# Optimization experiments

Measured on AMD Instinct MI355X. Metric: run time of the kernel, lower is better.

Reference implementation:

```python
import jax, jax.numpy as jnp
import numpy as np

ALPHA = 2.0    # ATan surrogate sharpness
V_TH = 1.0     # LIF firing threshold
TAU = 2.0      # LIF membrane time constant
BN_EPS = 1e-5
NUM_HEADS = 8

@jax.custom_vjp
def spike(u):
    return (u >= 0.0).astype(u.dtype)

def _spike_fwd(u):
    return spike(u), u

def _spike_bwd(u, g):
    s = (jnp.pi / 2.0) * ALPHA * u
    return (g * (ALPHA / 2.0) / (1.0 + s * s),)

spike.defvjp(_spike_fwd, _spike_bwd)

def lif(x):
    # x: (T, ...) -> binary spikes, multi-step LIF with hard reset
    def step(mem, xt):
        mem = mem + (xt - mem) / TAU
        s = spike(mem - V_TH)
        return mem * (1.0 - s), s
    _, out = jax.lax.scan(step, jnp.zeros_like(x[0]), x)
    return out

def bn_eval(y, bn):
    g, be, m, v = bn[0], bn[1], bn[2], bn[3]  # each (C,)
    return (y - m) * jax.lax.rsqrt(v + BN_EPS) * g + be

def linear_bn_lif(x, W, b, bn):
    # x: (T,B,N,C); W: (C_out, C_in) torch convention
    y = jnp.einsum('tbnc,dc->tbnd', x, W) + b
    return lif(bn_eval(y, bn))

def setup_inputs() -> dict:
    key = jax.random.key(0)
    ks = jax.random.split(key, 6)
    T, B, N, C = 4, 8, 1024, 512
    scale = 1.0 / np.sqrt(C)
    x = jax.random.normal(ks[0], (T, B, N, C), dtype=jnp.float32)
    Wq = jax.random.normal(ks[1], (C, C), dtype=jnp.float32) * scale
    Wk = jax.random.normal(ks[2], (C, C), dtype=jnp.float32) * scale
    Wv = jax.random.normal(ks[3], (C, C), dtype=jnp.float32) * scale
    Wp = jax.random.normal(ks[4], (C, C), dtype=jnp.float32) * scale
    zeros = jnp.zeros((C,), dtype=jnp.float32)
    ones = jnp.ones((C,), dtype=jnp.float32)
    # bn_params[l] = (gamma, beta, running_mean, running_var) for q_bn,k_bn,v_bn,proj_bn
    bn_one = jnp.stack([ones, zeros, zeros, ones])  # (4, C)
    bn_params = jnp.tile(bn_one[None], (4, 1, 1))   # (4, 4, C)
    return {"x": x, "Wq": Wq, "bq": zeros, "Wk": Wk, "bk": zeros,
            "Wv": Wv, "bv": zeros, "Wp": Wp, "bp": zeros, "bn_params": bn_params}

def reference(x, Wq, bq, Wk, bk, Wv, bv, Wp, bp, bn_params):
    T, B, N, C = x.shape
    H = NUM_HEADS
    D = C // H
    q = linear_bn_lif(x, Wq, bq, bn_params[0])
    k = linear_bn_lif(x, Wk, bk, bn_params[1])
    v = linear_bn_lif(x, Wv, bv, bn_params[2])
    # (T,B,N,C) -> (T,B,H,N,D)
    q = q.reshape(T, B, N, H, D).transpose(0, 1, 3, 2, 4)
    k = k.reshape(T, B, N, H, D).transpose(0, 1, 3, 2, 4)
    v = v.reshape(T, B, N, H, D).transpose(0, 1, 3, 2, 4)
    # attention_linear variant: kv = (k^T @ v) / n; y = q @ kv
    # SparseMatmul's tile-sparsity fallback computes the same dense matmul math.
    kv = jnp.einsum('tbhnd,tbhne->tbhde', k, v) / float(N)
    y = jnp.einsum('tbhnd,tbhde->tbhne', q, kv)
    y = y.transpose(0, 1, 3, 2, 4).reshape(T, B, N, C)
    y = lif(y)  # attn_lif
    # final projection: proj -> proj_bn -> proj_lif
    y = jnp.einsum('tbnc,dc->tbnd', y, Wp) + bp
    y = bn_eval(y, bn_params[3])
    y = lif(y)  # proj_lif
    return y
```

## Files before the change

### kernel.cpp

```cpp
#include <hip/hip_runtime.h>
#include <hip/hip_bf16.h>

constexpr int T_ = 4, B_ = 8, N_ = 1024, C_ = 512, H_ = 8, D_ = 64;
constexpr int M_ = 8192;
constexpr int MT_ = 32768;
constexpr int K_ = 512;

#define TAU_INV 0.5f
#define V_TH    1.0f
#define BN_EPS  1e-5f

__device__ __forceinline__ void ld4(const float* p, float* d) {
  const float4 v = *(const float4*)p;
  d[0] = v.x; d[1] = v.y; d[2] = v.z; d[3] = v.w;
}
__device__ __forceinline__ void ld4(const __hip_bfloat16* p, float* d) {
  const ushort4 u = *(const ushort4*)p;
  d[0] = __bfloat162float(*(const __hip_bfloat16*)&u.x);
  d[1] = __bfloat162float(*(const __hip_bfloat16*)&u.y);
  d[2] = __bfloat162float(*(const __hip_bfloat16*)&u.z);
  d[3] = __bfloat162float(*(const __hip_bfloat16*)&u.w);
}
__device__ __forceinline__ void st4(__hip_bfloat16* p, const float* s) {
  ushort4 u;
  *(__hip_bfloat16*)&u.x = __float2bfloat16(s[0]);
  *(__hip_bfloat16*)&u.y = __float2bfloat16(s[1]);
  *(__hip_bfloat16*)&u.z = __float2bfloat16(s[2]);
  *(__hip_bfloat16*)&u.w = __float2bfloat16(s[3]);
  *(ushort4*)p = u;
}
__device__ __forceinline__ void st4(float* p, const float* s) {
  *(float4*)p = make_float4(s[0], s[1], s[2], s[3]);
}

__device__ __forceinline__ void dma16(const void* g, void* l) {
  __builtin_amdgcn_global_load_lds(
      (const __attribute__((address_space(1))) unsigned int*)g,
      (__attribute__((address_space(3))) unsigned int*)l, 16, 0, 0);
}

struct WPtrs { const float* W[4]; };

__global__ __launch_bounds__(256) void transpose_w(WPtrs wp, float* __restrict__ Wt)
{
  __shared__ float tile[32][33];
  const int w = blockIdx.z;
  const float* __restrict__ W = wp.W[w];
  float* __restrict__ dst = Wt + (size_t)w * K_ * C_;
  const int k0 = blockIdx.x * 32, d0 = blockIdx.y * 32;
  const int tx = threadIdx.x, ty = threadIdx.y;
#pragma unroll
  for (int i = 0; i < 32; i += 8)
    tile[ty + i][tx] = W[(size_t)(d0 + ty + i) * K_ + k0 + tx];
  __syncthreads();
#pragma unroll
  for (int i = 0; i < 32; i += 8)
    dst[(size_t)(k0 + ty + i) * C_ + d0 + tx] = tile[tx][ty + i];
}

__global__ __launch_bounds__(256) void transpose_x(
    const float* __restrict__ x, float* __restrict__ XT)
{
  __shared__ float tile[32][132];
  const int bk = blockIdx.x * 32, bm = blockIdx.y * 32;
  const int tx = threadIdx.x & 31, ty = threadIdx.x >> 5;
#pragma unroll
  for (int t = 0; t < T_; ++t)
#pragma unroll
    for (int i = 0; i < 4; ++i) {
      const int m = ty + 8 * i;
      tile[tx][m * 4 + t] = x[((size_t)t * M_ + bm + m) * K_ + bk + tx];
    }
  __syncthreads();
  const int k = threadIdx.x >> 3, q = threadIdx.x & 7;
#pragma unroll
  for (int u = 0; u < 4; ++u)
    st4(&XT[(size_t)(bk + k) * MT_ + bm * 4 + q * 16 + u * 4],
        &tile[k][q * 16 + u * 4]);
}

template <typename TIn, typename TOut>
struct GArgs {
  const TIn* AT;
  const float* Wt[3];
  const float* bias[3];
  const float* bn[3];
  TOut* S[3];
};

template <typename TIn, typename TOut>
__global__ __launch_bounds__(256, 2) void gemm_lif(GArgs<TIn, TOut> args)
{
  constexpr int BK = 32;
  constexpr bool BF = (sizeof(TIn) == 2);
  __shared__ __align__(16) TIn  As[BK * 128];
  __shared__ __align__(16) float Bs[BK * 256];

  const int z = blockIdx.z;
  const TIn*   __restrict__ AT   = args.AT;
  const float* __restrict__ Wt   = args.Wt[z];
  const float* __restrict__ bias = args.bias[z];
  const float* __restrict__ bnp  = args.bn[z];
  TOut*        __restrict__ S    = args.S[z];

  const int tid  = threadIdx.x;
  const int lane = tid & 63;
  const int wave = __builtin_amdgcn_readfirstlane(tid >> 6);
  const int tx = tid & 15, ty = tid >> 4;
  const int bm_m = blockIdx.y * 32;
  const int bm4  = bm_m * 4;
  const int bn0  = blockIdx.x * 256;

  float acc[2][4][4][4];
#pragma unroll
  for (int g = 0; g < 2; ++g)
#pragma unroll
    for (int h = 0; h < 4; ++h)
#pragma unroll
      for (int i = 0; i < 4; ++i)
#pragma unroll
        for (int j = 0; j < 4; ++j) acc[g][h][i][j] = 0.0f;

  for (int k0 = 0; k0 < K_; k0 += BK) {
    if constexpr (!BF) {
#pragma unroll
      for (int c = 0; c < 4; ++c) {
        const int ins = wave * 4 + c;
        const int kk = ins * 2 + (lane >> 5);
        dma16(AT + (size_t)(k0 + kk) * MT_ + bm4 + (lane & 31) * 4,
              (void*)((float*)As + ins * 256));
      }
    } else {
#pragma unroll
      for (int c = 0; c < 2; ++c) {
        const int ins = wave * 2 + c;
        const int kk = ins * 4 + (lane >> 4);
        dma16(AT + (size_t)(k0 + kk) * MT_ + bm4 + (lane & 15) * 8,
              (void*)((TIn*)As + ins * 512));
      }
    }
#pragma unroll
    for (int c = 0; c < 8; ++c) {
      const int ins = wave * 8 + c;
      dma16(Wt + (size_t)(k0 + ins) * C_ + bn0 + lane * 4,
            (void*)(Bs + ins * 256));
    }
    __syncthreads();

#pragma unroll
    for (int kk = 0; kk < BK; ++kk) {
      float a[2][4], b[4][4];
#pragma unroll
      for (int g = 0; g < 2; ++g)
        ld4((const TIn*)As + kk * 128 + ty * 4 + 64 * g, a[g]);
#pragma unroll
      for (int h = 0; h < 4; ++h)
        ld4(Bs + kk * 256 + tx * 4 + 64 * h, b[h]);
#pragma unroll
      for (int g = 0; g < 2; ++g)
#pragma unroll
        for (int h = 0; h < 4; ++h)
#pragma unroll
          for (int i = 0; i < 4; ++i)
#pragma unroll
            for (int j = 0; j < 4; ++j)
              acc[g][h][i][j] += a[g][i] * b[h][j];
    }
    __syncthreads();
  }

#pragma unroll
  for (int h = 0; h < 4; ++h) {
    const int d = bn0 + tx * 4 + 64 * h;
    float bi[4], gg[4], be[4], mu[4], vv[4];
    ld4(&bias[d], bi);
    ld4(&bnp[d], gg);
    ld4(&bnp[C_ + d], be);
    ld4(&bnp[2 * C_ + d], mu);
    ld4(&bnp[3 * C_ + d], vv);
    float inv[4];
#pragma unroll
    for (int j = 0; j < 4; ++j) inv[j] = 1.0f / sqrtf(vv[j] + BN_EPS);
#pragma unroll
    for (int g = 0; g < 2; ++g) {
      const int m = bm_m + ty + 16 * g;
      float sv[4][4];
#pragma unroll
      for (int j = 0; j < 4; ++j) {
        float mm = 0.0f;
#pragma unroll
        for (int t = 0; t < 4; ++t) {
          float y = acc[g][h][t][j] + bi[j];
          y = (y - mu[j]) * inv[j] * gg[j] + be[j];
          float m2 = mm + (y - mm) * TAU_INV;
          float s = (m2 - V_TH >= 0.0f) ? 1.0f : 0.0f;
          sv[t][j] = s;
          mm = (s != 0.0f) ? 0.0f : m2;
        }
      }
#pragma unroll
      for (int t = 0; t < 4; ++t)
        st4(&S[((size_t)t * M_ + m) * C_ + d], sv[t]);
    }
  }
}

__global__ __launch_bounds__(256) void lif_T(
    const float* __restrict__ Y, __hip_bfloat16* __restrict__ AT)
{
  __shared__ __hip_bfloat16 lds[64][72];
  const int bm = blockIdx.x * 16, bc = blockIdx.y * 64;
  const int tid = threadIdx.x;
  const int mm = tid >> 4, c4 = (tid & 15) * 4;
  float mem[4] = {0.0f, 0.0f, 0.0f, 0.0f};
#pragma unroll
  for (int t = 0; t < T_; ++t) {
    float y[4];
    ld4(&Y[((size_t)t * M_ + bm + mm) * C_ + bc + c4], y);
#pragma unroll
    for (int j = 0; j < 4; ++j) {
      float m2 = mem[j] + (y[j] - mem[j]) * TAU_INV;
      float s = (m2 - V_TH >= 0.0f) ? 1.0f : 0.0f;
      lds[c4 + j][mm * 4 + t] = __float2bfloat16(s);
      mem[j] = (s != 0.0f) ? 0.0f : m2;
    }
  }
  __syncthreads();
  const int c = tid >> 2, q = tid & 3;
  *(uint4*)(AT + (size_t)(bc + c) * MT_ + bm * 4 + q * 16) =
      *(const uint4*)&lds[c][q * 16];
}

__global__ __launch_bounds__(256) void attn_kernel(
    const __hip_bfloat16* __restrict__ Q,
    const __hip_bfloat16* __restrict__ Kk,
    const __hip_bfloat16* __restrict__ V,
    float* __restrict__ Y)
{
  __shared__ float s1[64][65];
  __shared__ float s2[64][65];
  __shared__ float kv[64][65];
  const int tid = threadIdx.x;
  const int h = blockIdx.x, b = blockIdx.y, t = blockIdx.z;
  const size_t base = ((size_t)t * B_ + b) * (size_t)N_ * C_ + (size_t)h * D_;
  const int d0 = (tid >> 4) * 4;
  const int e0 = (tid & 15) * 4;

  float acc[4][4];
#pragma unroll
  for (int i = 0; i < 4; ++i)
#pragma unroll
    for (int j = 0; j < 4; ++j) acc[i][j] = 0.0f;

  for (int nc = 0; nc < N_; nc += 64) {
#pragma unroll
    for (int i = 0; i < 16; ++i) {
      int idx = tid + i * 256;
      int r = idx >> 6, c = idx & 63;
      s1[r][c] = __bfloat162float(Kk[base + (size_t)(nc + r) * C_ + c]);
      s2[r][c] = __bfloat162float(V[base + (size_t)(nc + r) * C_ + c]);
    }
    __syncthreads();
#pragma unroll
    for (int nn = 0; nn < 64; ++nn) {
      float a[4], bb[4];
#pragma unroll
      for (int i = 0; i < 4; ++i) a[i] = s1[nn][d0 + i];
#pragma unroll
      for (int j = 0; j < 4; ++j) bb[j] = s2[nn][e0 + j];
#pragma unroll
      for (int i = 0; i < 4; ++i)
#pragma unroll
        for (int j = 0; j < 4; ++j) acc[i][j] += a[i] * bb[j];
    }
    __syncthreads();
  }
#pragma unroll
  for (int i = 0; i < 4; ++i)
#pragma unroll
    for (int j = 0; j < 4; ++j)
      kv[d0 + i][e0 + j] = acc[i][j] * (1.0f / (float)N_);
  __syncthreads();

  for (int rc = 0; rc < N_; rc += 64) {
#pragma unroll
    for (int i = 0; i < 16; ++i) {
      int idx = tid + i * 256;
      int r = idx >> 6, c = idx & 63;
      s1[r][c] = __bfloat162float(Q[base + (size_t)(rc + r) * C_ + c]);
    }
    __syncthreads();
    float o[4][4];
#pragma unroll
    for (int i = 0; i < 4; ++i)
#pragma unroll
      for (int j = 0; j < 4; ++j) o[i][j] = 0.0f;
#pragma unroll
    for (int d = 0; d < 64; ++d) {
      float a[4], bb[4];
#pragma unroll
      for (int i = 0; i < 4; ++i) a[i] = s1[d0 + i][d];
#pragma unroll
      for (int j = 0; j < 4; ++j) bb[j] = kv[d][e0 + j];
#pragma unroll
      for (int i = 0; i < 4; ++i)
#pragma unroll
        for (int j = 0; j < 4; ++j) o[i][j] += a[i] * bb[j];
    }
#pragma unroll
    for (int i = 0; i < 4; ++i)
#pragma unroll
      for (int j = 0; j < 4; ++j)
        Y[base + (size_t)(rc + d0 + i) * C_ + e0 + j] = o[i][j];
    __syncthreads();
  }
}

extern "C" void kernel_launch(void* const* d_in, const int* in_sizes, int n_in,
                              void* d_out, int out_size, void* d_ws, size_t ws_size,
                              hipStream_t stream)
{
  const float* x   = (const float*)d_in[0];
  const float* Wq  = (const float*)d_in[1];
  const float* bq  = (const float*)d_in[2];
  const float* Wk  = (const float*)d_in[3];
  const float* bk  = (const float*)d_in[4];
  const float* Wv  = (const float*)d_in[5];
  const float* bv  = (const float*)d_in[6];
  const float* Wp  = (const float*)d_in[7];
  const float* bp  = (const float*)d_in[8];
  const float* bnp = (const float*)d_in[9];
  float* out = (float*)d_out;

  char* ws = (char*)d_ws;
  float* XT = (float*)ws;  ws += (size_t)K_ * MT_ * sizeof(float);
  float* Wt = (float*)ws;  ws += (size_t)4 * K_ * C_ * sizeof(float);
  __hip_bfloat16* q_s = (__hip_bfloat16*)ws; ws += (size_t)MT_ * C_ * 2;
  __hip_bfloat16* k_s = (__hip_bfloat16*)ws; ws += (size_t)MT_ * C_ * 2;
  __hip_bfloat16* v_s = (__hip_bfloat16*)ws; ws += (size_t)MT_ * C_ * 2;
  float* Y = XT;
  __hip_bfloat16* aT = q_s;

  WPtrs wp; wp.W[0] = Wq; wp.W[1] = Wk; wp.W[2] = Wv; wp.W[3] = Wp;
  transpose_w<<<dim3(K_ / 32, C_ / 32, 4), dim3(32, 8), 0, stream>>>(wp, Wt);
  transpose_x<<<dim3(K_ / 32, M_ / 32), 256, 0, stream>>>(x, XT);

  GArgs<float, __hip_bfloat16> qa;
  qa.AT = XT;
  qa.Wt[0] = Wt; qa.Wt[1] = Wt + (size_t)K_ * C_; qa.Wt[2] = Wt + (size_t)2 * K_ * C_;
  qa.bias[0] = bq; qa.bias[1] = bk; qa.bias[2] = bv;
  qa.bn[0] = bnp + 0 * 4 * C_;
  qa.bn[1] = bnp + 1 * 4 * C_;
  qa.bn[2] = bnp + 2 * 4 * C_;
  qa.S[0] = q_s; qa.S[1] = k_s; qa.S[2] = v_s;
  gemm_lif<float, __hip_bfloat16>
      <<<dim3(C_ / 256, M_ / 32, 3), 256, 0, stream>>>(qa);

  attn_kernel<<<dim3(H_, B_, T_), 256, 0, stream>>>(q_s, k_s, v_s, Y);
  lif_T<<<dim3(M_ / 16, C_ / 64), 256, 0, stream>>>(Y, aT);

  GArgs<__hip_bfloat16, float> pa;
  pa.AT = aT;
  pa.Wt[0] = Wt + (size_t)3 * K_ * C_;
  pa.bias[0] = bp;
  pa.bn[0] = bnp + 3 * 4 * C_;
  pa.S[0] = out;
  gemm_lif<__hip_bfloat16, float>
      <<<dim3(C_ / 256, M_ / 32, 1), 256, 0, stream>>>(pa);
}
```

Before: 992.7 us.

## Split attention into KV-partial kernel and fused q@kv+LIF+transpose kernel

Replaces the single attention kernel and the separate LIF-transpose pass with two kernels. The first computes per-wave partial k^T v products, loading tiles into LDS via direct global-to-LDS DMA, and writes four partial sums. The second sums the partials, multiplies them by Q tiles over all timesteps, and applies the attention LIF in registers, so it writes bf16 spikes straight in the transposed layout. This removes the fp32 Y round trip through memory and raises parallelism for the q@kv stage, at the cost of a small partial-sum buffer and extra reduction work per block.

```diff
diff --git a/kernel.cpp b/kernel.cpp
--- a/kernel.cpp
+++ b/kernel.cpp
@@ -20,6 +20,13 @@
   d[1] = __bfloat162float(*(const __hip_bfloat16*)&u.y);
   d[2] = __bfloat162float(*(const __hip_bfloat16*)&u.z);
   d[3] = __bfloat162float(*(const __hip_bfloat16*)&u.w);
+}
+__device__ __forceinline__ void ld8bf(const __hip_bfloat16* p, float* d) {
+  union { uint4 u; ushort s[8]; } q;
+  q.u = *(const uint4*)p;
+#pragma unroll
+  for (int j = 0; j < 8; ++j)
+    d[j] = __bfloat162float(*(const __hip_bfloat16*)&q.s[j]);
 }
 __device__ __forceinline__ void st4(__hip_bfloat16* p, const float* s) {
   ushort4 u;
@@ -205,114 +212,168 @@
   }
 }
 
-__global__ __launch_bounds__(256) void lif_T(
-    const float* __restrict__ Y, __hip_bfloat16* __restrict__ AT)
-{
-  __shared__ __hip_bfloat16 lds[64][72];
-  const int bm = blockIdx.x * 16, bc = blockIdx.y * 64;
-  const int tid = threadIdx.x;
-  const int mm = tid >> 4, c4 = (tid & 15) * 4;
-  float mem[4] = {0.0f, 0.0f, 0.0f, 0.0f};
-#pragma unroll
-  for (int t = 0; t < T_; ++t) {
-    float y[4];
-    ld4(&Y[((size_t)t * M_ + bm + mm) * C_ + bc + c4], y);
-#pragma unroll
-    for (int j = 0; j < 4; ++j) {
-      float m2 = mem[j] + (y[j] - mem[j]) * TAU_INV;
-      float s = (m2 - V_TH >= 0.0f) ? 1.0f : 0.0f;
-      lds[c4 + j][mm * 4 + t] = __float2bfloat16(s);
-      mem[j] = (s != 0.0f) ? 0.0f : m2;
-    }
-  }
-  __syncthreads();
-  const int c = tid >> 2, q = tid & 3;
-  *(uint4*)(AT + (size_t)(bc + c) * MT_ + bm * 4 + q * 16) =
-      *(const uint4*)&lds[c][q * 16];
-}
-
-__global__ __launch_bounds__(256) void attn_kernel(
-    const __hip_bfloat16* __restrict__ Q,
+__global__ __launch_bounds__(256) void kv_kernel(
     const __hip_bfloat16* __restrict__ Kk,
     const __hip_bfloat16* __restrict__ V,
-    float* __restrict__ Y)
-{
-  __shared__ float s1[64][65];
-  __shared__ float s2[64][65];
-  __shared__ float kv[64][65];
-  const int tid = threadIdx.x;
+    float* __restrict__ kvpT)
+{
+  __shared__ __align__(16) __hip_bfloat16 Ks[64 * 64];
+  __shared__ __align__(16) __hip_bfloat16 Vs[64 * 64];
+  const int tid  = threadIdx.x;
+  const int lane = tid & 63;
+  const int w    = __builtin_amdgcn_readfirstlane(tid >> 6);
   const int h = blockIdx.x, b = blockIdx.y, t = blockIdx.z;
-  const size_t base = ((size_t)t * B_ + b) * (size_t)N_ * C_ + (size_t)h * D_;
-  const int d0 = (tid >> 4) * 4;
-  const int e0 = (tid & 15) * 4;
-
-  float acc[4][4];
-#pragma unroll
-  for (int i = 0; i < 4; ++i)
-#pragma unroll
-    for (int j = 0; j < 4; ++j) acc[i][j] = 0.0f;
+  const size_t base = ((size_t)(t * B_ + b) * N_) * C_ + (size_t)h * D_;
+  const int d0 = (lane >> 3) * 8;
+  const int e0 = (lane & 7) * 8;
+
+  float acc[8][8];
+#pragma unroll
+  for (int i = 0; i < 8; ++i)
+#pragma unroll
+    for (int j = 0; j < 8; ++j) acc[i][j] = 0.0f;
 
   for (int nc = 0; nc < N_; nc += 64) {
 #pragma unroll
-    for (int i = 0; i < 16; ++i) {
-      int idx = tid + i * 256;
-      int r = idx >> 6, c = idx & 63;
-      s1[r][c] = __bfloat162float(Kk[base + (size_t)(nc + r) * C_ + c]);
-      s2[r][c] = __bfloat162float(V[base + (size_t)(nc + r) * C_ + c]);
+    for (int c = 0; c < 2; ++c) {
+      const int ins = w * 2 + c;
+      const int row = ins * 8 + (lane >> 3);
+      const int ch  = lane & 7;
+      dma16(Kk + base + (size_t)(nc + row) * C_ + ch * 8,
+            (void*)(Ks + ins * 512));
+      dma16(V  + base + (size_t)(nc + row) * C_ + ch * 8,
+            (void*)(Vs + ins * 512));
     }
     __syncthreads();
 #pragma unroll
-    for (int nn = 0; nn < 64; ++nn) {
-      float a[4], bb[4];
-#pragma unroll
-      for (int i = 0; i < 4; ++i) a[i] = s1[nn][d0 + i];
-#pragma unroll
-      for (int j = 0; j < 4; ++j) bb[j] = s2[nn][e0 + j];
-#pragma unroll
-      for (int i = 0; i < 4; ++i)
-#pragma unroll
-        for (int j = 0; j < 4; ++j) acc[i][j] += a[i] * bb[j];
+    for (int s = 0; s < 16; ++s) {
+      const int nn = w * 16 + s;
+      float a[8], bb[8];
+      ld8bf(Ks + nn * 64 + d0, a);
+      ld8bf(Vs + nn * 64 + e0, bb);
+#pragma unroll
+      for (int i = 0; i < 8; ++i)
+#pragma unroll
+        for (int j = 0; j < 8; ++j) acc[i][j] += a[i] * bb[j];
     }
     __syncthreads();
   }
-#pragma unroll
-  for (int i = 0; i < 4; ++i)
-#pragma unroll
-    for (int j = 0; j < 4; ++j)
-      kv[d0 + i][e0 + j] = acc[i][j] * (1.0f / (float)N_);
-  __syncthreads();
-
-  for (int rc = 0; rc < N_; rc += 64) {
-#pragma unroll
-    for (int i = 0; i < 16; ++i) {
-      int idx = tid + i * 256;
-      int r = idx >> 6, c = idx & 63;
-      s1[r][c] = __bfloat162float(Q[base + (size_t)(rc + r) * C_ + c]);
+
+  float* dst = kvpT + ((((size_t)t * B_ + b) * H_ + h) * 4 + w) * (size_t)(D_ * D_);
+#pragma unroll
+  for (int j = 0; j < 8; ++j) {
+    float tmp[8];
+#pragma unroll
+    for (int i = 0; i < 8; ++i) tmp[i] = acc[i][j];
+    st4(&dst[(e0 + j) * D_ + d0], tmp);
+    st4(&dst[(e0 + j) * D_ + d0 + 4], tmp + 4);
+  }
+}
+
+__device__ __forceinline__ unsigned bfpair(unsigned bits, int j, int half) {
+  const unsigned p = (bits >> (j * 4 + half * 2)) & 3u;
+  return ((p & 1u) ? 0x3F80u : 0u) | ((p & 2u) ? 0x3F800000u : 0u);
+}
+
+__global__ __launch_bounds__(256, 2) void attn_y(
+    const __hip_bfloat16* __restrict__ Q,
+    const float* __restrict__ kvpT,
+    __hip_bfloat16* __restrict__ AT)
+{
+  __shared__ __align__(16) __hip_bfloat16 Qs[128 * 64];
+  __shared__ __align__(16) float KVs[64][68];
+  const int tid  = threadIdx.x;
+  const int lane = tid & 63;
+  const int w    = __builtin_amdgcn_readfirstlane(tid >> 6);
+  const int n0 = blockIdx.x * 128;
+  const int h  = blockIdx.y, b = blockIdx.z;
+  const int ng = lane & 15;
+  const int e0 = w * 16 + (lane >> 4) * 4;
+
+  float mem[8][4];
+  unsigned svb[8];
+#pragma unroll
+  for (int i = 0; i < 8; ++i) {
+    svb[i] = 0u;
+#pragma unroll
+    for (int j = 0; j < 4; ++j) mem[i][j] = 0.0f;
+  }
+
+#pragma unroll
+  for (int t = 0; t < T_; ++t) {
+    if (t) __syncthreads();
+#pragma unroll
+    for (int c = 0; c < 4; ++c) {
+      const int ins = w * 4 + c;
+      const int row = ins * 8 + (lane >> 3);
+      const int ch  = (lane & 7) ^ (ins & 7);
+      dma16(Q + (size_t)(t * M_ + b * N_ + n0 + row) * C_ + h * D_ + ch * 8,
+            (void*)(Qs + ins * 512));
+    }
+    const float* kp = kvpT + (((size_t)t * B_ + b) * H_ + h) * 4 * (size_t)(D_ * D_);
+#pragma unroll
+    for (int g = 0; g < 4; ++g) {
+      const int cell = tid * 16 + g * 4;
+      const float4 v0 = *(const float4*)(kp + cell);
+      const float4 v1 = *(const float4*)(kp + 4096 + cell);
+      const float4 v2 = *(const float4*)(kp + 8192 + cell);
+      const float4 v3 = *(const float4*)(kp + 12288 + cell);
+      float sum[4] = { v0.x + v1.x + v2.x + v3.x, v0.y + v1.y + v2.y + v3.y,
+                       v0.z + v1.z + v2.z + v3.z, v0.w + v1.w + v2.w + v3.w };
+      st4(&KVs[cell >> 6][cell & 63], sum);
     }
     __syncthreads();
-    float o[4][4];
-#pragma unroll
-    for (int i = 0; i < 4; ++i)
-#pragma unroll
-      for (int j = 0; j < 4; ++j) o[i][j] = 0.0f;
-#pragma unroll
-    for (int d = 0; d < 64; ++d) {
-      float a[4], bb[4];
-#pragma unroll
-      for (int i = 0; i < 4; ++i) a[i] = s1[d0 + i][d];
-#pragma unroll
-      for (int j = 0; j < 4; ++j) bb[j] = kv[d][e0 + j];
-#pragma unroll
-      for (int i = 0; i < 4; ++i)
-#pragma unroll
-        for (int j = 0; j < 4; ++j) o[i][j] += a[i] * bb[j];
-    }
-#pragma unroll
-    for (int i = 0; i < 4; ++i)
-#pragma unroll
-      for (int j = 0; j < 4; ++j)
-        Y[base + (size_t)(rc + d0 + i) * C_ + e0 + j] = o[i][j];
-    __syncthreads();
+
+    float acc[8][4];
+#pragma unroll
+    for (int i = 0; i < 8; ++i)
+#pragma unroll
+      for (int j = 0; j < 4; ++j) acc[i][j] = 0.0f;
+#pragma unroll 2
+    for (int dc = 0; dc < 8; ++dc) {
+      float bb[4][8];
+#pragma unroll
+      for (int j = 0; j < 4; ++j) {
+        ld4(&KVs[e0 + j][dc * 8], bb[j]);
+        ld4(&KVs[e0 + j][dc * 8 + 4], bb[j] + 4);
+      }
+#pragma unroll
+      for (int i = 0; i < 8; ++i) {
+        float a[8];
+        ld8bf(Qs + (ng * 8 + i) * 64 + ((dc ^ (ng & 7)) * 8), a);
+#pragma unroll
+        for (int dd = 0; dd < 8; ++dd)
+#pragma unroll
+          for (int j = 0; j < 4; ++j)
+            acc[i][j] += a[dd] * bb[j][dd];
+      }
+    }
+
+#pragma unroll
+    for (int i = 0; i < 8; ++i)
+#pragma unroll
+      for (int j = 0; j < 4; ++j) {
+        const float y = acc[i][j] * 0.0009765625f;
+        const float m2 = mem[i][j] + (y - mem[i][j]) * TAU_INV;
+        const float s = (m2 - V_TH >= 0.0f) ? 1.0f : 0.0f;
+        if (s != 0.0f) svb[i] |= 1u << (j * 4 + t);
+        mem[i][j] = (s != 0.0f) ? 0.0f : m2;
+      }
+  }
+
+  const size_t mbase = ((size_t)b * N_ + n0 + ng * 8) * 4;
+#pragma unroll
+  for (int j = 0; j < 4; ++j) {
+    __hip_bfloat16* dst = AT + (size_t)(h * D_ + e0 + j) * MT_ + mbase;
+#pragma unroll
+    for (int p = 0; p < 4; ++p) {
+      uint4 u;
+      u.x = bfpair(svb[2 * p],     j, 0);
+      u.y = bfpair(svb[2 * p],     j, 1);
+      u.z = bfpair(svb[2 * p + 1], j, 0);
+      u.w = bfpair(svb[2 * p + 1], j, 1);
+      *(uint4*)(dst + p * 8) = u;
+    }
   }
 }
 
@@ -338,8 +399,8 @@
   __hip_bfloat16* q_s = (__hip_bfloat16*)ws; ws += (size_t)MT_ * C_ * 2;
   __hip_bfloat16* k_s = (__hip_bfloat16*)ws; ws += (size_t)MT_ * C_ * 2;
   __hip_bfloat16* v_s = (__hip_bfloat16*)ws; ws += (size_t)MT_ * C_ * 2;
-  float* Y = XT;
-  __hip_bfloat16* aT = q_s;
+  __hip_bfloat16* aT = (__hip_bfloat16*)XT;
+  float* kvpT = (float*)((char*)XT + (size_t)32 * 1024 * 1024);
 
   WPtrs wp; wp.W[0] = Wq; wp.W[1] = Wk; wp.W[2] = Wv; wp.W[3] = Wp;
   transpose_w<<<dim3(K_ / 32, C_ / 32, 4), dim3(32, 8), 0, stream>>>(wp, Wt);
@@ -356,8 +417,8 @@
   gemm_lif<float, __hip_bfloat16>
       <<<dim3(C_ / 256, M_ / 32, 3), 256, 0, stream>>>(qa);
 
-  attn_kernel<<<dim3(H_, B_, T_), 256, 0, stream>>>(q_s, k_s, v_s, Y);
-  lif_T<<<dim3(M_ / 16, C_ / 64), 256, 0, stream>>>(Y, aT);
+  kv_kernel<<<dim3(H_, B_, T_), 256, 0, stream>>>(k_s, v_s, kvpT);
+  attn_y<<<dim3(N_ / 128, H_, B_), 256, 0, stream>>>(q_s, kvpT, aT);
 
   GArgs<__hip_bfloat16, float> pa;
   pa.AT = aT;
```

Result: slower. 1.099 ms (+10.7%).
